# Performance work log

Hardware: AMD Instinct MI355X
Metric: run time of the kernel (lower is better)

## Reference

```python
import jax, jax.numpy as jnp
import numpy as np

N_NODES = 100000
N_EDGES = 3200000
F_IN = 256
H = 128


def setup_inputs() -> dict:
    key = jax.random.key(0)
    ks = jax.random.split(key, 7)
    x = jax.random.normal(ks[0], (N_NODES, F_IN), dtype=jnp.float32)
    edge_row = jax.random.randint(ks[1], (N_EDGES,), 0, N_NODES, dtype=jnp.int32)
    edge_col = jax.random.randint(ks[2], (N_EDGES,), 0, N_NODES, dtype=jnp.int32)
    edge_val = jax.random.uniform(ks[3], (N_EDGES,), dtype=jnp.float32)
    # Glorot-ish scaled weights (Dense: F_IN->H, two GCN layers: H->H)
    W_dense = jax.random.normal(ks[4], (F_IN, H), dtype=jnp.float32) / np.sqrt(F_IN)
    W_gcn1 = jax.random.normal(ks[5], (H, H), dtype=jnp.float32) / np.sqrt(H)
    W_gcn2 = jax.random.normal(ks[6], (H, H), dtype=jnp.float32) / np.sqrt(H)
    return {"x": x, "edge_row": edge_row, "edge_col": edge_col, "edge_val": edge_val,
            "W_dense": W_dense, "W_gcn1": W_gcn1, "W_gcn2": W_gcn2}


def _gcn_layer(edge_row, edge_col, edge_val, h, W):
    # support = h @ W  (dense GEMM), then sparse adjacency matmul: A @ support
    support = h @ W                                   # [N, H]
    msgs = edge_val[:, None] * support[edge_col]      # gather source nodes, weight by adj values
    agg = jax.ops.segment_sum(msgs, edge_row, num_segments=N_NODES)  # scatter-add to destinations
    return jax.nn.relu(agg)


def reference(x, edge_row, edge_col, edge_val, W_dense, W_gcn1, W_gcn2):
    # Dense layer: act(x @ W)
    h = jax.nn.relu(x @ W_dense)                      # [N, H]
    # Stacked GraphConvolution layers: act(A @ (h @ W))
    h = _gcn_layer(edge_row, edge_col, edge_val, h, W_gcn1)
    h = _gcn_layer(edge_row, edge_col, edge_val, h, W_gcn2)
    return h
```

## Files before the change

### kernel.cpp

```cpp
#include <hip/hip_runtime.h>
#include <hip/hip_fp16.h>

static constexpr int NN  = 100000;
static constexpr int NE  = 3200000;
static constexpr int FIN = 256;
static constexpr int HD  = 128;

static constexpr int NB    = 400;
static constexpr int BROWS = 250;
static constexpr int BCAP  = 10000;
static constexpr int DCAP  = 9000;
static constexpr int CHUNK = 4096;

using half8 = __attribute__((ext_vector_type(8))) _Float16;
using f32x4 = __attribute__((ext_vector_type(4))) float;
using f32x2 = __attribute__((ext_vector_type(2))) float;

__global__ __launch_bounds__(256)
void wt_convert_all(const float* __restrict__ Wd, const float* __restrict__ W1,
                    const float* __restrict__ W2, _Float16* __restrict__ WtD,
                    _Float16* __restrict__ Wt1, _Float16* __restrict__ Wt2) {
    int i = blockIdx.x * 256 + threadIdx.x;
    if (i < FIN * HD) {
        int k = i >> 7, c = i & 127;
        WtD[c * FIN + k] = (_Float16)Wd[i];
    }
    if (i < HD * HD) {
        int k = i >> 7, c = i & 127;
        Wt1[c * HD + k] = (_Float16)W1[i];
        Wt2[c * HD + k] = (_Float16)W2[i];
    }
}

template<int K, bool A_F16, bool RELU_OUT, bool OUT_FP8>
__global__ __launch_bounds__(256)
void mfma_gemm(const void* __restrict__ Ain, const _Float16* __restrict__ Wt,
               void* __restrict__ Cout, int n) {
    __shared__ _Float16 As[64][40];
    __shared__ _Float16 Bs[128][40];
    const int t = threadIdx.x;
    const int lane = t & 63;
    const int w = t >> 6;
    const int row0 = blockIdx.x * 64;
    f32x4 acc[8];
#pragma unroll
    for (int i = 0; i < 8; ++i) acc[i] = {0.f, 0.f, 0.f, 0.f};

    const int ar = t >> 2;
    const int ak = (t & 3) * 8;
    const int bc = t & 127;
    const int bk = (t >> 7) * 16;

    for (int k0 = 0; k0 < K; k0 += 32) {
        {
            const int grow = row0 + ar;
            half8 h = {};
            if (grow < n) {
                if (A_F16) {
                    h = *reinterpret_cast<const half8*>(
                        (const _Float16*)Ain + (size_t)grow * K + k0 + ak);
                } else {
                    const float* Af = (const float*)Ain;
                    float4 v0 = *reinterpret_cast<const float4*>(Af + (size_t)grow * K + k0 + ak);
                    float4 v1 = *reinterpret_cast<const float4*>(Af + (size_t)grow * K + k0 + ak + 4);
                    h[0] = (_Float16)v0.x; h[1] = (_Float16)v0.y;
                    h[2] = (_Float16)v0.z; h[3] = (_Float16)v0.w;
                    h[4] = (_Float16)v1.x; h[5] = (_Float16)v1.y;
                    h[6] = (_Float16)v1.z; h[7] = (_Float16)v1.w;
                }
            }
            *reinterpret_cast<half8*>(&As[ar][ak]) = h;
        }
        *reinterpret_cast<half8*>(&Bs[bc][bk]) =
            *reinterpret_cast<const half8*>(&Wt[(size_t)bc * K + k0 + bk]);
        *reinterpret_cast<half8*>(&Bs[bc][bk + 8]) =
            *reinterpret_cast<const half8*>(&Wt[(size_t)bc * K + k0 + bk + 8]);
        __syncthreads();

        half8 af = *reinterpret_cast<const half8*>(&As[16 * w + (lane & 15)][(lane >> 4) * 8]);
#pragma unroll
        for (int nt = 0; nt < 8; ++nt) {
            half8 bf = *reinterpret_cast<const half8*>(&Bs[16 * nt + (lane & 15)][(lane >> 4) * 8]);
            acc[nt] = __builtin_amdgcn_mfma_f32_16x16x32_f16(af, bf, acc[nt], 0, 0, 0);
        }
        __syncthreads();
    }
    const int orow0 = row0 + 16 * w + (lane >> 4) * 4;
    const int ocol = lane & 15;
#pragma unroll
    for (int nt = 0; nt < 8; ++nt) {
#pragma unroll
        for (int q = 0; q < 4; ++q) {
            int r = orow0 + q;
            if (r < n) {
                float v = acc[nt][q];
                if (RELU_OUT) v = fmaxf(v, 0.f);
                if (OUT_FP8) {
                    int pk = __builtin_amdgcn_cvt_pk_fp8_f32(v, v, 0, false);
                    ((unsigned char*)Cout)[(size_t)r * HD + 16 * nt + ocol] =
                        (unsigned char)(pk & 0xFF);
                } else {
                    ((_Float16*)Cout)[(size_t)r * HD + 16 * nt + ocol] = (_Float16)v;
                }
            }
        }
    }
}

__global__ __launch_bounds__(512)
void bucket_init(int* __restrict__ bucketCursor, int* __restrict__ rowptr) {
    int t = threadIdx.x;
    if (t < NB) bucketCursor[t] = t * BCAP;
    if (t == 0) rowptr[NN] = NB * DCAP;
}

__global__ __launch_bounds__(512)
void bucket_bin(const int* __restrict__ erow, const int* __restrict__ ecol,
                const float* __restrict__ eval, int* __restrict__ bucketCursor,
                int2* __restrict__ stage) {
    __shared__ int bcnt[NB];
    __shared__ int offx[512];
    __shared__ int goff[NB];
    __shared__ int2 st[CHUNK];
    int* sc = (int*)st;

    const int t = threadIdx.x;
    const long base = (long)blockIdx.x * CHUNK;
    const int total = (int)min((long)CHUNK, (long)NE - base);

    if (t < NB) bcnt[t] = 0;
    __syncthreads();

    int key[8], val[8], rkb[8];
#pragma unroll
    for (int i = 0; i < 8; ++i) {
        long e = base + t + i * 512;
        if (e < NE) {
            int row = erow[e];
            int col = ecol[e];
            int b = row / BROWS;
            int lr = row - b * BROWS;
            key[i] = (lr << 17) | col;
            val[i] = __float_as_int(eval[e]);
            int rk = atomicAdd(&bcnt[b], 1);
            rkb[i] = (rk << 9) | b;
        } else { rkb[i] = -1; key[i] = 0; val[i] = 0; }
    }
    __syncthreads();

    int v = (t < NB) ? bcnt[t] : 0;
    sc[t] = v;
    __syncthreads();
    for (int off = 1; off < 512; off <<= 1) {
        int x = sc[t];
        int add = (t >= off) ? sc[t - off] : 0;
        __syncthreads();
        sc[t] = x + add;
        __syncthreads();
    }
    offx[t] = sc[t] - v;
    if (t < NB && v > 0) goff[t] = atomicAdd(&bucketCursor[t], v);
    __syncthreads();

#pragma unroll
    for (int i = 0; i < 8; ++i) {
        if (rkb[i] >= 0) {
            int b  = rkb[i] & 511;
            int rk = rkb[i] >> 9;
            st[offx[b] + rk] = make_int2(key[i], val[i]);
        }
    }
    __syncthreads();

    for (int s = t; s < total; s += 512) {
        int lo = 0, hi = NB - 1;
        while (lo < hi) {
            int mid = (lo + hi + 1) >> 1;
            if (offx[mid] <= s) lo = mid; else hi = mid - 1;
        }
        stage[goff[lo] + (s - offx[lo])] = st[s];
    }
}

__global__ __launch_bounds__(512)
void bucket_to_csr(const int2* __restrict__ stage, const int* __restrict__ bucketCursor,
                   int* __restrict__ rowptr, int2* __restrict__ csr) {
    __shared__ int2 dst[DCAP];
    __shared__ int  lh[256];
    __shared__ int  lcur[BROWS];

    const int b = blockIdx.x;
    const int t = threadIdx.x;
    const long sbase = (long)b * BCAP;
    const int n = bucketCursor[b] - b * BCAP;

    if (t < 256) lh[t] = 0;
    for (int i = t; i < DCAP; i += 512) dst[i] = make_int2(0, 0);
    __syncthreads();

    for (int i = t; i < n; i += 512)
        atomicAdd(&lh[((unsigned)stage[sbase + i].x) >> 17], 1);
    __syncthreads();

    int p = 0;
    if (t < 256) { p = (lh[t] + 3) & ~3; lh[t] = p; }
    __syncthreads();
    for (int off = 1; off < 256; off <<= 1) {
        int x = 0, add = 0;
        if (t < 256) { x = lh[t]; add = (t >= off) ? lh[t - off] : 0; }
        __syncthreads();
        if (t < 256) lh[t] = x + add;
        __syncthreads();
    }
    if (t < BROWS) {
        int excl = lh[t] - p;
        lcur[t] = excl;
        rowptr[b * BROWS + t] = b * DCAP + excl;
    }
    __syncthreads();

    for (int i = t; i < n; i += 512) {
        int2 kv = stage[sbase + i];
        int lr  = ((unsigned)kv.x) >> 17;
        int col = kv.x & 0x1FFFF;
        int pos = atomicAdd(&lcur[lr], 1);
        if (pos < DCAP) dst[pos] = make_int2(col, kv.y);
    }
    __syncthreads();

    const long gb = (long)b * DCAP;
    for (int i = t; i < DCAP; i += 512) csr[gb + i] = dst[i];
}

template<bool OUT_F32>
__global__ __launch_bounds__(256)
void pull_oct(const int* __restrict__ rowptr, const int2* __restrict__ csr,
              const unsigned char* __restrict__ S8, void* __restrict__ out) {
    const int row  = (blockIdx.x * 256 + threadIdx.x) >> 6;
    const int lane = threadIdx.x & 63;
    const int g    = lane >> 3;
    const int s    = lane & 7;
    if (row >= NN) return;

    int p = rowptr[row];
    const int p1 = rowptr[row + 1];
    f32x2 acc2[8];
#pragma unroll
    for (int j = 0; j < 8; ++j) acc2[j] = {0.f, 0.f};

    auto fma16 = [&](uint4 w, float v) {
        const f32x2 vv = {v, v};
        acc2[0] = __builtin_elementwise_fma(vv, __builtin_amdgcn_cvt_pk_f32_fp8(w.x, false), acc2[0]);
        acc2[1] = __builtin_elementwise_fma(vv, __builtin_amdgcn_cvt_pk_f32_fp8(w.x, true),  acc2[1]);
        acc2[2] = __builtin_elementwise_fma(vv, __builtin_amdgcn_cvt_pk_f32_fp8(w.y, false), acc2[2]);
        acc2[3] = __builtin_elementwise_fma(vv, __builtin_amdgcn_cvt_pk_f32_fp8(w.y, true),  acc2[3]);
        acc2[4] = __builtin_elementwise_fma(vv, __builtin_amdgcn_cvt_pk_f32_fp8(w.z, false), acc2[4]);
        acc2[5] = __builtin_elementwise_fma(vv, __builtin_amdgcn_cvt_pk_f32_fp8(w.z, true),  acc2[5]);
        acc2[6] = __builtin_elementwise_fma(vv, __builtin_amdgcn_cvt_pk_f32_fp8(w.w, false), acc2[6]);
        acc2[7] = __builtin_elementwise_fma(vv, __builtin_amdgcn_cvt_pk_f32_fp8(w.w, true),  acc2[7]);
    };

    for (; p + 16 <= p1; p += 16) {
        int2 kv0 = csr[p + g];
        int2 kv1 = csr[p + 8 + g];
        uint4 w0 = *reinterpret_cast<const uint4*>(S8 + (size_t)kv0.x * HD + s * 16);
        uint4 w1 = *reinterpret_cast<const uint4*>(S8 + (size_t)kv1.x * HD + s * 16);
        fma16(w0, __int_as_float(kv0.y));
        fma16(w1, __int_as_float(kv1.y));
    }
    for (; p < p1; p += 8) {
        const bool a = (p + g) < p1;
        int2 kv = a ? csr[p + g] : make_int2(0, 0);
        uint4 w = *reinterpret_cast<const uint4*>(S8 + (size_t)kv.x * HD + s * 16);
        fma16(w, a ? __int_as_float(kv.y) : 0.f);
    }

    float acc[16];
#pragma unroll
    for (int j = 0; j < 8; ++j) { acc[2 * j] = acc2[j][0]; acc[2 * j + 1] = acc2[j][1]; }
#pragma unroll
    for (int j = 0; j < 16; ++j) {
        acc[j] += __shfl_xor(acc[j], 8);
        acc[j] += __shfl_xor(acc[j], 16);
        acc[j] += __shfl_xor(acc[j], 32);
        acc[j] = fmaxf(acc[j], 0.f);
    }

    if (g == 0) {
        if (OUT_F32) {
            float* o = (float*)out + (size_t)row * HD + s * 16;
            *reinterpret_cast<float4*>(o)      = make_float4(acc[0],  acc[1],  acc[2],  acc[3]);
            *reinterpret_cast<float4*>(o + 4)  = make_float4(acc[4],  acc[5],  acc[6],  acc[7]);
            *reinterpret_cast<float4*>(o + 8)  = make_float4(acc[8],  acc[9],  acc[10], acc[11]);
            *reinterpret_cast<float4*>(o + 12) = make_float4(acc[12], acc[13], acc[14], acc[15]);
        } else {
            _Float16* o = (_Float16*)out + (size_t)row * HD + s * 16;
            half8 h0, h1;
#pragma unroll
            for (int j = 0; j < 8; ++j) { h0[j] = (_Float16)acc[j]; h1[j] = (_Float16)acc[8 + j]; }
            *reinterpret_cast<half8*>(o)     = h0;
            *reinterpret_cast<half8*>(o + 8) = h1;
        }
    }
}

extern "C" void kernel_launch(void* const* d_in, const int* in_sizes, int n_in,
                              void* d_out, int out_size, void* d_ws, size_t ws_size,
                              hipStream_t stream) {
    const float* x    = (const float*)d_in[0];
    const int*   erow = (const int*)d_in[1];
    const int*   ecol = (const int*)d_in[2];
    const float* eval = (const float*)d_in[3];
    const float* Wd   = (const float*)d_in[4];
    const float* W1   = (const float*)d_in[5];
    const float* W2   = (const float*)d_in[6];
    float* out = (float*)d_out;

    const size_t bufElems = (size_t)NN * HD;
    _Float16*      hbuf  = (_Float16*)d_ws;
    unsigned char* sbuf  = (unsigned char*)(hbuf + bufElems);
    int2*          stage = (int2*)d_ws;
    int2*          csr   = (int2*)(sbuf + bufElems);
    _Float16*      WtD   = (_Float16*)(csr + (size_t)NB * DCAP);
    _Float16*      Wt1   = WtD + (size_t)FIN * HD;
    _Float16*      Wt2   = Wt1 + (size_t)HD * HD;
    int* rowptr       = (int*)(Wt2 + (size_t)HD * HD);
    int* bucketCursor = rowptr + (NN + 1);

    const int gemmBlocks = (NN + 63) / 64;
    const int binBlocks  = (NE + CHUNK - 1) / CHUNK;
    const int pullBlocks = (NN * 64 + 255) / 256;

    bucket_init<<<1, 512, 0, stream>>>(bucketCursor, rowptr);
    bucket_bin<<<binBlocks, 512, 0, stream>>>(erow, ecol, eval, bucketCursor, stage);
    bucket_to_csr<<<NB, 512, 0, stream>>>(stage, bucketCursor, rowptr, csr);

    wt_convert_all<<<(FIN * HD + 255) / 256, 256, 0, stream>>>(Wd, W1, W2, WtD, Wt1, Wt2);

    mfma_gemm<FIN, false, true, false><<<gemmBlocks, 256, 0, stream>>>(x, WtD, hbuf, NN);
    mfma_gemm<HD, true, false, true><<<gemmBlocks, 256, 0, stream>>>(hbuf, Wt1, sbuf, NN);
    pull_oct<false><<<pullBlocks, 256, 0, stream>>>(rowptr, csr, sbuf, hbuf);
    mfma_gemm<HD, true, false, true><<<gemmBlocks, 256, 0, stream>>>(hbuf, Wt2, sbuf, NN);
    pull_oct<true><<<pullBlocks, 256, 0, stream>>>(rowptr, csr, sbuf, out);
}
```

Baseline: 287.3 us.

## Fuse dense layer GEMM and first GCN support GEMM into one kernel

Chains the x@W_dense GEMM with ReLU and the h@W_gcn1 GEMM inside one kernel. The intermediate 64x128 tile stays in shared memory as fp16 instead of being written to and re-read from global memory. This saves one kernel launch and the round trip of the N x 128 intermediate buffer. In exchange it adds LDS per block (about 17KB extra), which may lower occupancy, and the epilogue stores FP8 outputs with scalar byte writes.

```diff
diff --git a/kernel.cpp b/kernel.cpp
--- a/kernel.cpp
+++ b/kernel.cpp
@@ -29,6 +29,102 @@
         int k = i >> 7, c = i & 127;
         Wt1[c * HD + k] = (_Float16)W1[i];
         Wt2[c * HD + k] = (_Float16)W2[i];
+    }
+}
+
+__global__ __launch_bounds__(256)
+void gemm_fused12(const float* __restrict__ X, const _Float16* __restrict__ WtD,
+                  const _Float16* __restrict__ Wt1, unsigned char* __restrict__ Cout,
+                  int n) {
+    __shared__ _Float16 As[64][40];
+    __shared__ _Float16 Bs[128][40];
+    __shared__ _Float16 As2[64][136];
+    const int t = threadIdx.x;
+    const int lane = t & 63;
+    const int w = t >> 6;
+    const int row0 = blockIdx.x * 64;
+    f32x4 acc[8];
+#pragma unroll
+    for (int i = 0; i < 8; ++i) acc[i] = {0.f, 0.f, 0.f, 0.f};
+
+    const int ar = t >> 2;
+    const int ak = (t & 3) * 8;
+    const int bc = t & 127;
+    const int bk = (t >> 7) * 16;
+
+    for (int k0 = 0; k0 < FIN; k0 += 32) {
+        {
+            const int grow = row0 + ar;
+            half8 h = {};
+            if (grow < n) {
+                float4 v0 = *reinterpret_cast<const float4*>(X + (size_t)grow * FIN + k0 + ak);
+                float4 v1 = *reinterpret_cast<const float4*>(X + (size_t)grow * FIN + k0 + ak + 4);
+                h[0] = (_Float16)v0.x; h[1] = (_Float16)v0.y;
+                h[2] = (_Float16)v0.z; h[3] = (_Float16)v0.w;
+                h[4] = (_Float16)v1.x; h[5] = (_Float16)v1.y;
+                h[6] = (_Float16)v1.z; h[7] = (_Float16)v1.w;
+            }
+            *reinterpret_cast<half8*>(&As[ar][ak]) = h;
+        }
+        *reinterpret_cast<half8*>(&Bs[bc][bk]) =
+            *reinterpret_cast<const half8*>(&WtD[(size_t)bc * FIN + k0 + bk]);
+        *reinterpret_cast<half8*>(&Bs[bc][bk + 8]) =
+            *reinterpret_cast<const half8*>(&WtD[(size_t)bc * FIN + k0 + bk + 8]);
+        __syncthreads();
+
+        half8 af = *reinterpret_cast<const half8*>(&As[16 * w + (lane & 15)][(lane >> 4) * 8]);
+#pragma unroll
+        for (int nt = 0; nt < 8; ++nt) {
+            half8 bf = *reinterpret_cast<const half8*>(&Bs[16 * nt + (lane & 15)][(lane >> 4) * 8]);
+            acc[nt] = __builtin_amdgcn_mfma_f32_16x16x32_f16(af, bf, acc[nt], 0, 0, 0);
+        }
+        __syncthreads();
+    }
+
+    {
+        const int trow0 = 16 * w + (lane >> 4) * 4;
+        const int tcol  = lane & 15;
+#pragma unroll
+        for (int nt = 0; nt < 8; ++nt) {
+#pragma unroll
+            for (int q = 0; q < 4; ++q) {
+                As2[trow0 + q][16 * nt + tcol] = (_Float16)fmaxf(acc[nt][q], 0.f);
+            }
+            acc[nt] = {0.f, 0.f, 0.f, 0.f};
+        }
+    }
+    __syncthreads();
+
+    for (int k0 = 0; k0 < HD; k0 += 32) {
+        *reinterpret_cast<half8*>(&Bs[bc][bk]) =
+            *reinterpret_cast<const half8*>(&Wt1[(size_t)bc * HD + k0 + bk]);
+        *reinterpret_cast<half8*>(&Bs[bc][bk + 8]) =
+            *reinterpret_cast<const half8*>(&Wt1[(size_t)bc * HD + k0 + bk + 8]);
+        __syncthreads();
+
+        half8 af = *reinterpret_cast<const half8*>(
+            &As2[16 * w + (lane & 15)][k0 + (lane >> 4) * 8]);
+#pragma unroll
+        for (int nt = 0; nt < 8; ++nt) {
+            half8 bf = *reinterpret_cast<const half8*>(&Bs[16 * nt + (lane & 15)][(lane >> 4) * 8]);
+            acc[nt] = __builtin_amdgcn_mfma_f32_16x16x32_f16(af, bf, acc[nt], 0, 0, 0);
+        }
+        __syncthreads();
+    }
+
+    const int orow0 = row0 + 16 * w + (lane >> 4) * 4;
+    const int ocol = lane & 15;
+#pragma unroll
+    for (int nt = 0; nt < 8; ++nt) {
+#pragma unroll
+        for (int q = 0; q < 4; ++q) {
+            int r = orow0 + q;
+            if (r < n) {
+                float v = acc[nt][q];
+                int pk = __builtin_amdgcn_cvt_pk_fp8_f32(v, v, 0, false);
+                Cout[(size_t)r * HD + 16 * nt + ocol] = (unsigned char)(pk & 0xFF);
+            }
+        }
     }
 }
 
@@ -337,8 +433,7 @@
 
     wt_convert_all<<<(FIN * HD + 255) / 256, 256, 0, stream>>>(Wd, W1, W2, WtD, Wt1, Wt2);
 
-    mfma_gemm<FIN, false, true, false><<<gemmBlocks, 256, 0, stream>>>(x, WtD, hbuf, NN);
-    mfma_gemm<HD, true, false, true><<<gemmBlocks, 256, 0, stream>>>(hbuf, Wt1, sbuf, NN);
+    gemm_fused12<<<gemmBlocks, 256, 0, stream>>>(x, WtD, Wt1, sbuf, NN);
     pull_oct<false><<<pullBlocks, 256, 0, stream>>>(rowptr, csr, sbuf, hbuf);
     mfma_gemm<HD, true, false, true><<<gemmBlocks, 256, 0, stream>>>(hbuf, Wt2, sbuf, NN);
     pull_oct<true><<<pullBlocks, 256, 0, stream>>>(rowptr, csr, sbuf, out);
```

Measured after the change: 278.4 us. 3.1% less time.
